# Kernel optimization log

Hardware: AMD Instinct MI355X
Metric: run time of the kernel (lower is better)

The kernel has to match this reference:

```python
import jax, jax.numpy as jnp
import numpy as np

H = 16          # attention_head_num
DH = 64         # attention_head_size
D = H * DH      # out_dim / model dim
SIZE_PER_HEAD = 64  # scaling denominator (init arg, used as sqrt divisor)


def setup_inputs() -> dict:
    key = jax.random.key(0)
    ks = jax.random.split(key, 12)
    B, S = 2, 2048
    scale = 1.0 / np.sqrt(D)
    inp = {
        "qx": jax.random.normal(ks[0], (B, S, D), dtype=jnp.float32),
        "kx": jax.random.normal(ks[1], (B, S, D), dtype=jnp.float32),
        "vx": jax.random.normal(ks[2], (B, S, D), dtype=jnp.float32),
        "Wq": jax.random.normal(ks[3], (D, D), dtype=jnp.float32) * scale,
        "bq": jnp.zeros((D,), dtype=jnp.float32),
        "Wk": jax.random.normal(ks[4], (D, D), dtype=jnp.float32) * scale,
        "bk": jnp.zeros((D,), dtype=jnp.float32),
        "Wv": jax.random.normal(ks[5], (D, D), dtype=jnp.float32) * scale,
        "bv": jnp.zeros((D,), dtype=jnp.float32),
        "Wo": jax.random.normal(ks[6], (D, D), dtype=jnp.float32) * scale,
        "bo": jnp.zeros((D,), dtype=jnp.float32),
    }
    return inp


def reference(qx, kx, vx, Wq, bq, Wk, bk, Wv, bv, Wo, bo):
    B, Sq, _ = qx.shape
    Sk = kx.shape[1]
    # QKV projections
    q = qx @ Wq + bq  # [B,Sq,D]
    k = kx @ Wk + bk  # [B,Sk,D]
    v = vx @ Wv + bv  # [B,Sk,D]
    # split heads -> [B,H,S,DH]
    q = q.reshape(B, Sq, H, DH).transpose(0, 2, 1, 3)
    k = k.reshape(B, Sk, H, DH).transpose(0, 2, 1, 3)
    v = v.reshape(B, Sk, H, DH).transpose(0, 2, 1, 3)
    # scores [B,H,Sq,Sk]; NOTE: original divides by sqrt(size_per_head)
    scores = jnp.einsum("bhqd,bhkd->bhqk", q, k) / jnp.sqrt(
        jnp.asarray(SIZE_PER_HEAD, dtype=q.dtype)
    )
    probs = jax.nn.softmax(scores, axis=-1)
    ctx = jnp.einsum("bhqk,bhkd->bhqd", probs, v)  # [B,H,Sq,DH]
    ctx = ctx.transpose(0, 2, 1, 3).reshape(B, Sq, D)
    return ctx @ Wo + bo
```

## Files before the change

kernel.cpp:

```cpp
#include <hip/hip_runtime.h>

typedef _Float16 half_t;
typedef _Float16 half8 __attribute__((ext_vector_type(8)));
typedef _Float16 half2v __attribute__((ext_vector_type(2)));
typedef __fp16 fp16x2 __attribute__((ext_vector_type(2)));
typedef float f32x16 __attribute__((ext_vector_type(16)));
typedef float f32x4v __attribute__((ext_vector_type(4)));
typedef unsigned uint2v __attribute__((ext_vector_type(2)));

#define MFMA32(A, B, C) __builtin_amdgcn_mfma_f32_32x32x16_f16(A, B, C, 0, 0, 0)

#if __has_builtin(__builtin_amdgcn_exp2f)
#define EXP2F(x) __builtin_amdgcn_exp2f(x)
#else
#define EXP2F(x) exp2f(x)
#endif

static constexpr int S = 2048;
static constexpr int D = 1024;
static constexpr float QSCALE = 0.18033688011112042f;


__device__ __forceinline__ void gload_lds16(const void* g, void* l) {
    __builtin_amdgcn_global_load_lds(
        (const __attribute__((address_space(1))) unsigned int*)g,
        (__attribute__((address_space(3))) unsigned int*)l, 16, 0, 0);
}

__global__ __launch_bounds__(256) void cvtw(
    const float* __restrict__ x0, const float* __restrict__ x1, const float* __restrict__ x2,
    const float* __restrict__ w0, const float* __restrict__ w1,
    const float* __restrict__ w2, const float* __restrict__ w3,
    half_t* __restrict__ o0, half_t* __restrict__ o1, half_t* __restrict__ o2,
    half_t* __restrict__ wt)
{
    __shared__ char sm[33280];
    int y = blockIdx.y;
    int t = threadIdx.x;
    if (y < 3) {
        float (*tile)[65] = (float(*)[65])sm;
        const float* src = (y == 0) ? x0 : (y == 1) ? x1 : x2;
        half_t* dst = (y == 0) ? o0 : (y == 1) ? o1 : o2;
        int mt = blockIdx.x >> 4, kt = blockIdx.x & 15;
        const float* sbase = src + (size_t)(mt * 128) * D + kt * 64;
        int rr = t >> 4, col = (t & 15) * 4;
#pragma unroll
        for (int p = 0; p < 8; ++p) {
            int row = rr + p * 16;
            f32x4v v = *(const f32x4v*)(sbase + (size_t)row * D + col);
            tile[row][col] = v[0]; tile[row][col + 1] = v[1];
            tile[row][col + 2] = v[2]; tile[row][col + 3] = v[3];
        }
        __syncthreads();
        int c = t >> 5, r0 = t & 31;
        half_t* dbase = dst + ((size_t)(mt * 16 + kt)) * 8192;
#pragma unroll
        for (int i = 0; i < 4; ++i) {
            int row = r0 + 32 * i;
            half8 h;
#pragma unroll
            for (int j = 0; j < 8; ++j) h[j] = (half_t)tile[row][c * 8 + j];
            *(half8*)(dbase + ((size_t)c * 128 + row) * 8) = h;
        }
    } else {
        float (*tile)[129] = (float(*)[129])sm;
        int w = blockIdx.x >> 7;
        const float* W = (w == 0) ? w0 : (w == 1) ? w1 : (w == 2) ? w2 : w3;
        int idx = blockIdx.x & 127;
        int nt = idx >> 4, kt = idx & 15;
        const float* sbase = W + (size_t)(kt * 64) * D + nt * 128;
        int kr = t >> 5, col = (t & 31) * 4;
#pragma unroll
        for (int p = 0; p < 8; ++p) {
            int k = kr + p * 8;
            f32x4v v = *(const f32x4v*)(sbase + (size_t)k * D + col);
            tile[k][col] = v[0]; tile[k][col + 1] = v[1];
            tile[k][col + 2] = v[2]; tile[k][col + 3] = v[3];
        }
        __syncthreads();
        int c = t >> 5, r0 = t & 31;
        half_t* dbase = wt + (size_t)w * 1048576 + ((size_t)(nt * 16 + kt)) * 8192;
#pragma unroll
        for (int i = 0; i < 4; ++i) {
            int n = r0 + 32 * i;
            half8 h;
#pragma unroll
            for (int j = 0; j < 8; ++j) h[j] = (half_t)tile[c * 8 + j][n];
            *(half8*)(dbase + ((size_t)c * 128 + n) * 8) = h;
        }
    }
}

__global__ __launch_bounds__(256, 4) void gemm_qkv(
    const half_t* __restrict__ a0, const half_t* __restrict__ a1, const half_t* __restrict__ a2,
    const half_t* __restrict__ wt,
    const float* __restrict__ b0, const float* __restrict__ b1, const float* __restrict__ b2,
    half_t* __restrict__ qh, half_t* __restrict__ kh, half_t* __restrict__ vt)
{
    __shared__ char smem[32768];
    half_t* As = (half_t*)smem;
    half_t* Bs = (half_t*)(smem + 16384);
    int z = blockIdx.z;
    const half_t* A = (z == 0) ? a0 : (z == 1) ? a1 : a2;
    const half_t* BT = wt + (size_t)z * 1048576;
    const float* bias = (z == 0) ? b0 : (z == 1) ? b1 : b2;
    int mt = blockIdx.x >> 3, nt8 = blockIdx.x & 7;
    int m0 = mt * 128, n0 = nt8 * 128;
    int tid = threadIdx.x, lane = tid & 63, wave = tid >> 6;
    int ml = lane & 31, hi = lane >> 5;
    int wm = (wave & 1) * 64, wn = (wave >> 1) * 64;

    f32x16 acc00 = {}, acc01 = {}, acc10 = {}, acc11 = {};

    for (int kt = 0; kt < 16; ++kt) {
        __syncthreads();
        const half_t* Aslab = A + ((size_t)(mt * 16 + kt)) * 8192;
        const half_t* Bslab = BT + ((size_t)(nt8 * 16 + kt)) * 8192;
#pragma unroll
        for (int j = 0; j < 4; ++j) {
            int s = wave * 4 + j;
            gload_lds16(Aslab + s * 512 + lane * 8, As + s * 512);
            gload_lds16(Bslab + s * 512 + lane * 8, Bs + s * 512);
        }
        __syncthreads();
#pragma unroll
        for (int ks = 0; ks < 4; ++ks) {
            int co = (2 * ks + hi) * 128;
            half8 af0 = *(const half8*)(As + (size_t)(co + wm + ml) * 8);
            half8 af1 = *(const half8*)(As + (size_t)(co + wm + 32 + ml) * 8);
            half8 bf0 = *(const half8*)(Bs + (size_t)(co + wn + ml) * 8);
            half8 bf1 = *(const half8*)(Bs + (size_t)(co + wn + 32 + ml) * 8);
            acc00 = MFMA32(af0, bf0, acc00);
            acc01 = MFMA32(af0, bf1, acc01);
            acc10 = MFMA32(af1, bf0, acc10);
            acc11 = MFMA32(af1, bf1, acc11);
        }
    }

    __syncthreads();
    half_t* buf = (half_t*)smem;
#pragma unroll
    for (int nt = 0; nt < 2; ++nt) {
        int nl = wn + nt * 32 + ml;
        float bv = bias[n0 + nl];
        int hh = nl >> 6, c = (nl >> 3) & 7, j = nl & 7, dd = nl & 63;
#pragma unroll
        for (int mt2 = 0; mt2 < 2; ++mt2) {
            f32x16 av = (mt2 == 0) ? (nt == 0 ? acc00 : acc01) : (nt == 0 ? acc10 : acc11);
#pragma unroll
            for (int r = 0; r < 16; ++r) {
                int rl = wm + mt2 * 32 + 4 * hi + (r & 3) + 8 * (r >> 2);
                float v = av[r] + bv;
                if (z == 0) v *= QSCALE;
                if (z <= 1) {
                    buf[((rl * 2 + hh) * 8 + (c ^ (rl & 7))) * 8 + j] = (half_t)v;
                } else {
                    int cc = rl >> 3, js = rl & 7;
                    buf[((dd * 2 + hh) * 16 + (cc ^ (dd & 7))) * 8 + js] = (half_t)v;
                }
            }
        }
    }
    __syncthreads();
    int bq_ = m0 >> 11, skt = (m0 >> 7) & 15, h0 = n0 >> 6;
    half_t* dstm = (z == 0) ? qh : (z == 1) ? kh : vt;
#pragma unroll
    for (int i = 0; i < 8; ++i) {
        int o = tid + 256 * i;
        int hh = o >> 10;
        half_t* gdst = dstm + ((size_t)(bq_ * 16 + h0 + hh)) * 131072 + (size_t)skt * 8192;
        half8 v8;
        int off;
        if (z <= 1) {
            int c = (o >> 7) & 7, r = o & 127;
            v8 = *(const half8*)(buf + (((r * 2 + hh) * 8 + (c ^ (r & 7))) * 8));
            off = (c * 128 + r) * 8;
        } else {
            int cc = (o >> 6) & 15, dd = o & 63;
            v8 = *(const half8*)(buf + (((dd * 2 + hh) * 16 + (cc ^ (dd & 7))) * 8));
            off = (cc * 64 + dd) * 8;
        }
        *(half8*)(gdst + off) = v8;
    }
}

__global__ __launch_bounds__(256, 4) void gemm_out(
    const half_t* __restrict__ A, const half_t* __restrict__ BT,
    const float* __restrict__ bias, float* __restrict__ out)
{
    __shared__ char smem[32768];
    half_t* As = (half_t*)smem;
    half_t* Bs = (half_t*)(smem + 16384);
    int mt = blockIdx.x >> 3, nt8 = blockIdx.x & 7;
    int m0 = mt * 128, n0 = nt8 * 128;
    int tid = threadIdx.x, lane = tid & 63, wave = tid >> 6;
    int ml = lane & 31, hi = lane >> 5;
    int wm = (wave & 1) * 64, wn = (wave >> 1) * 64;

    f32x16 acc00 = {}, acc01 = {}, acc10 = {}, acc11 = {};

    for (int kt = 0; kt < 16; ++kt) {
        __syncthreads();
        const half_t* Aslab = A + ((size_t)(mt * 16 + kt)) * 8192;
        const half_t* Bslab = BT + ((size_t)(nt8 * 16 + kt)) * 8192;
#pragma unroll
        for (int j = 0; j < 4; ++j) {
            int s = wave * 4 + j;
            gload_lds16(Aslab + s * 512 + lane * 8, As + s * 512);
            gload_lds16(Bslab + s * 512 + lane * 8, Bs + s * 512);
        }
        __syncthreads();
#pragma unroll
        for (int ks = 0; ks < 4; ++ks) {
            int co = (2 * ks + hi) * 128;
            half8 af0 = *(const half8*)(As + (size_t)(co + wm + ml) * 8);
            half8 af1 = *(const half8*)(As + (size_t)(co + wm + 32 + ml) * 8);
            half8 bf0 = *(const half8*)(Bs + (size_t)(co + wn + ml) * 8);
            half8 bf1 = *(const half8*)(Bs + (size_t)(co + wn + 32 + ml) * 8);
            acc00 = MFMA32(af0, bf0, acc00);
            acc01 = MFMA32(af0, bf1, acc01);
            acc10 = MFMA32(af1, bf0, acc10);
            acc11 = MFMA32(af1, bf1, acc11);
        }
    }

#pragma unroll
    for (int nt = 0; nt < 2; ++nt) {
        int n = n0 + wn + nt * 32 + ml;
        float bv = bias[n];
#pragma unroll
        for (int mt2 = 0; mt2 < 2; ++mt2) {
            f32x16 av = (mt2 == 0) ? (nt == 0 ? acc00 : acc01) : (nt == 0 ? acc10 : acc11);
            int rbase = m0 + wm + mt2 * 32 + 4 * hi;
#pragma unroll
            for (int r = 0; r < 16; ++r) {
                int row = rbase + (r & 3) + 8 * (r >> 2);
                out[(size_t)row * D + n] = av[r] + bv;
            }
        }
    }
}

__global__ __launch_bounds__(256, 2) void attn(
    const half_t* __restrict__ qh, const half_t* __restrict__ kh,
    const half_t* __restrict__ vt, half_t* __restrict__ ctx)
{
    __shared__ char smem[32768];
    half_t* Ks  = (half_t*)smem;
    half_t* VTs = (half_t*)(smem + 16384);

    int L = blockIdx.x;
    int slot = L >> 3;
    int bh = (L & 7) + 8 * (slot >> 4);
    int sq = slot & 15;
    int b = bh >> 4, h = bh & 15;

    int tid = threadIdx.x, lane = tid & 63, wave = tid >> 6;
    int ml = lane & 31, hi = lane >> 5;
    int qg = wave & 1, th = wave >> 1;
    const half_t* qslab = qh + (size_t)bh * 131072 + (size_t)sq * 8192;
    const half_t* khead = kh + (size_t)bh * 131072;
    const half_t* vhead = vt + (size_t)bh * 131072;

#pragma unroll
    for (int j = 0; j < 4; ++j) {
        int s = wave * 4 + j;
        gload_lds16(qslab + s * 512 + lane * 8, Ks + s * 512);
    }
    __syncthreads();
    half8 qf[2][4];
#pragma unroll
    for (int qs = 0; qs < 2; ++qs)
#pragma unroll
        for (int ks = 0; ks < 4; ++ks)
            qf[qs][ks] = *(const half8*)(Ks + ((size_t)((2 * ks + hi) * 128 + qg * 64 + qs * 32 + ml)) * 8);

    f32x16 oacc[2][2] = {};
    float lsum[2] = {0.0f, 0.0f};
    fp16x2 one2; one2.x = (__fp16)1.0f; one2.y = (__fp16)1.0f;

    for (int it = 0; it < 16; ++it) {
        __syncthreads();
        const half_t* kslab = khead + (size_t)it * 8192;
        const half_t* vslab = vhead + (size_t)it * 8192;
#pragma unroll
        for (int j = 0; j < 4; ++j) {
            int s = wave * 4 + j;
            gload_lds16(kslab + s * 512 + lane * 8, Ks + s * 512);
            gload_lds16(vslab + s * 512 + lane * 8, VTs + s * 512);
        }
        __syncthreads();

#pragma unroll
        for (int tt = 0; tt < 2; ++tt) {
            int t = th * 2 + tt;
            f32x16 s0 = {}, s1 = {};
#pragma unroll
            for (int ks = 0; ks < 4; ++ks) {
                half8 kf = *(const half8*)(Ks + ((size_t)((2 * ks + hi) * 128 + t * 32 + ml)) * 8);
                s0 = MFMA32(kf, qf[0][ks], s0);
                s1 = MFMA32(kf, qf[1][ks], s1);
            }
#pragma unroll
            for (int qs = 0; qs < 2; ++qs) {
                f32x16 sv = (qs == 0) ? s0 : s1;
                unsigned pkv[8];
                float ls = lsum[qs];
#pragma unroll
                for (int j = 0; j < 8; ++j) {
                    float pa = EXP2F(sv[2 * j] - 10.0f);
                    float pb = EXP2F(sv[2 * j + 1] - 10.0f);
#if __has_builtin(__builtin_amdgcn_cvt_pkrtz)
                    fp16x2 h2 = __builtin_amdgcn_cvt_pkrtz(pa, pb);
#else
                    fp16x2 h2; h2.x = (__fp16)pa; h2.y = (__fp16)pb;
#endif
                    pkv[j] = __builtin_bit_cast(unsigned, h2);
#if __has_builtin(__builtin_amdgcn_fdot2)
                    ls = __builtin_amdgcn_fdot2(h2, one2, ls, false);
#else
                    ls += pa + pb;
#endif
                }
                lsum[qs] = ls;
#pragma unroll
                for (int kp = 0; kp < 2; ++kp) {
                    union { unsigned u[4]; half8 h; } fr;
#if __has_builtin(__builtin_amdgcn_permlane32_swap)
                    uint2v w0 = __builtin_amdgcn_permlane32_swap(pkv[4 * kp + 0], pkv[4 * kp + 2], false, false);
                    uint2v w1 = __builtin_amdgcn_permlane32_swap(pkv[4 * kp + 1], pkv[4 * kp + 3], false, false);
                    fr.u[0] = w0.x; fr.u[1] = w1.x; fr.u[2] = w0.y; fr.u[3] = w1.y;
#else
                    unsigned e0 = pkv[4 * kp + 0], e1 = pkv[4 * kp + 1];
                    unsigned o0 = pkv[4 * kp + 2], o1 = pkv[4 * kp + 3];
                    unsigned s0u = hi ? e0 : o0, s1u = hi ? e1 : o1;
                    unsigned k0u = hi ? o0 : e0, k1u = hi ? o1 : e1;
                    unsigned r0 = __shfl_xor(s0u, 32, 64);
                    unsigned r1 = __shfl_xor(s1u, 32, 64);
                    fr.u[0] = hi ? r0 : k0u; fr.u[1] = hi ? r1 : k1u;
                    fr.u[2] = hi ? k0u : r0; fr.u[3] = hi ? k1u : r1;
#endif
#pragma unroll
                    for (int dt = 0; dt < 2; ++dt) {
                        half8 vf = *(const half8*)(VTs + ((size_t)((4 * t + 2 * kp + hi) * 64 + dt * 32 + ml)) * 8);
                        oacc[qs][dt] = MFMA32(fr.h, vf, oacc[qs][dt]);
                    }
                }
            }
        }
    }

    float lt[2];
    lt[0] = lsum[0] + __shfl_xor(lsum[0], 32, 64);
    lt[1] = lsum[1] + __shfl_xor(lsum[1], 32, 64);

    __syncthreads();
    float* OB = (float*)(smem + (size_t)qg * 16384);
    if (th == 1) {
#pragma unroll
        for (int qs = 0; qs < 2; ++qs)
#pragma unroll
            for (int dt = 0; dt < 2; ++dt)
#pragma unroll
                for (int r = 0; r < 16; ++r) {
                    int q = qs * 32 + 4 * hi + (r & 3) + 8 * (r >> 2);
                    OB[q * 64 + dt * 32 + ml] = oacc[qs][dt][r];
                }
    }
    __syncthreads();
    if (th == 0) {
#pragma unroll
        for (int qs = 0; qs < 2; ++qs)
#pragma unroll
            for (int dt = 0; dt < 2; ++dt)
#pragma unroll
                for (int r = 0; r < 16; ++r) {
                    int q = qs * 32 + 4 * hi + (r & 3) + 8 * (r >> 2);
                    oacc[qs][dt][r] += OB[q * 64 + dt * 32 + ml];
                }
    }
    __syncthreads();
    float* Lbuf = (float*)smem;
    if (th == 1 && hi == 0) {
        Lbuf[qg * 64 + ml] = lt[0];
        Lbuf[qg * 64 + 32 + ml] = lt[1];
    }
    __syncthreads();
    if (th == 0 && hi == 0) {
        Lbuf[qg * 64 + ml] += lt[0];
        Lbuf[qg * 64 + 32 + ml] += lt[1];
    }
    __syncthreads();
    if (th == 0) {
        half_t* cslab = ctx + ((size_t)((b * 16 + sq) * 16 + h)) * 8192;
#pragma unroll
        for (int qs = 0; qs < 2; ++qs)
#pragma unroll
            for (int dt = 0; dt < 2; ++dt)
#pragma unroll
                for (int r = 0; r < 16; ++r) {
                    int q = qs * 32 + 4 * hi + (r & 3) + 8 * (r >> 2);
                    int d = dt * 32 + ml;
                    float linv = __builtin_amdgcn_rcpf(Lbuf[qg * 64 + q]);
                    cslab[((d >> 3) * 128 + qg * 64 + q) * 8 + (d & 7)] =
                        (half_t)(oacc[qs][dt][r] * linv);
                }
    }
}

extern "C" void kernel_launch(void* const* d_in, const int* in_sizes, int n_in,
                              void* d_out, int out_size, void* d_ws, size_t ws_size,
                              hipStream_t stream)
{
    const float* qx = (const float*)d_in[0];
    const float* kx = (const float*)d_in[1];
    const float* vx = (const float*)d_in[2];
    const float* Wq = (const float*)d_in[3];
    const float* bq = (const float*)d_in[4];
    const float* Wk = (const float*)d_in[5];
    const float* bk = (const float*)d_in[6];
    const float* Wv = (const float*)d_in[7];
    const float* bv = (const float*)d_in[8];
    const float* Wo = (const float*)d_in[9];
    const float* bo = (const float*)d_in[10];
    float* out = (float*)d_out;

    half_t* ws = (half_t*)d_ws;
    const size_t NT = (size_t)4096 * 1024;
    half_t* qxh = ws;
    half_t* kxh = qxh + NT;
    half_t* vxh = kxh + NT;
    half_t* wt = vxh + NT;
    half_t* qh = wt + (size_t)4 * 1048576;
    half_t* kh = qh + NT;
    half_t* vtr = kh + NT;
    half_t* ctx = vtr + NT;

    cvtw<<<dim3(512, 4), 256, 0, stream>>>(qx, kx, vx, Wq, Wk, Wv, Wo, qxh, kxh, vxh, wt);
    gemm_qkv<<<dim3(256, 1, 3), 256, 0, stream>>>(qxh, kxh, vxh, wt, bq, bk, bv, qh, kh, vtr);
    attn<<<dim3(512, 1, 1), 256, 0, stream>>>(qh, kh, vtr, ctx);
    gemm_out<<<dim3(256, 1, 1), 256, 0, stream>>>(ctx, wt + (size_t)3 * 1048576, bo, out);
}
```

Measured before the change: 227.5 us.

## Double-buffer K/V tiles in attention and swizzle GEMM block order

The attention kernel now uses 64KB of LDS to double-buffer K and V tiles. The loads for the next key tile are issued before computing on the current one, and one barrier per iteration replaces two. Q gets its own LDS region, and the first K/V tile is loaded together with it. Both GEMM kernels also remap block indices so that consecutive blocks share B column tiles and spread across M, aiming for better L2 reuse; the larger LDS footprint may limit occupancy.

```diff
diff --git a/kernel.cpp b/kernel.cpp
--- a/kernel.cpp
+++ b/kernel.cpp
@@ -2,7 +2,6 @@
 
 typedef _Float16 half_t;
 typedef _Float16 half8 __attribute__((ext_vector_type(8)));
-typedef _Float16 half2v __attribute__((ext_vector_type(2)));
 typedef __fp16 fp16x2 __attribute__((ext_vector_type(2)));
 typedef float f32x16 __attribute__((ext_vector_type(16)));
 typedef float f32x4v __attribute__((ext_vector_type(4)));
@@ -104,7 +103,10 @@
     const half_t* A = (z == 0) ? a0 : (z == 1) ? a1 : a2;
     const half_t* BT = wt + (size_t)z * 1048576;
     const float* bias = (z == 0) ? b0 : (z == 1) ? b1 : b2;
-    int mt = blockIdx.x >> 3, nt8 = blockIdx.x & 7;
+    int L = blockIdx.x;
+    int w = L >> 3;
+    int mt = (L & 7) * 4 + (w & 3);
+    int nt8 = w >> 2;
     int m0 = mt * 128, n0 = nt8 * 128;
     int tid = threadIdx.x, lane = tid & 63, wave = tid >> 6;
     int ml = lane & 31, hi = lane >> 5;
@@ -191,7 +193,10 @@
     __shared__ char smem[32768];
     half_t* As = (half_t*)smem;
     half_t* Bs = (half_t*)(smem + 16384);
-    int mt = blockIdx.x >> 3, nt8 = blockIdx.x & 7;
+    int L = blockIdx.x;
+    int w = L >> 3;
+    int mt = (L & 7) * 4 + (w & 3);
+    int nt8 = w >> 2;
     int m0 = mt * 128, n0 = nt8 * 128;
     int tid = threadIdx.x, lane = tid & 63, wave = tid >> 6;
     int ml = lane & 31, hi = lane >> 5;
@@ -245,15 +250,13 @@
     const half_t* __restrict__ qh, const half_t* __restrict__ kh,
     const half_t* __restrict__ vt, half_t* __restrict__ ctx)
 {
-    __shared__ char smem[32768];
-    half_t* Ks  = (half_t*)smem;
-    half_t* VTs = (half_t*)(smem + 16384);
+    __shared__ char smem[65536];
 
     int L = blockIdx.x;
     int slot = L >> 3;
     int bh = (L & 7) + 8 * (slot >> 4);
     int sq = slot & 15;
-    int b = bh >> 4, h = bh & 15;
+    int b_ = bh >> 4, h = bh & 15;
 
     int tid = threadIdx.x, lane = tid & 63, wave = tid >> 6;
     int ml = lane & 31, hi = lane >> 5;
@@ -262,34 +265,50 @@
     const half_t* khead = kh + (size_t)bh * 131072;
     const half_t* vhead = vt + (size_t)bh * 131072;
 
-#pragma unroll
-    for (int j = 0; j < 4; ++j) {
-        int s = wave * 4 + j;
-        gload_lds16(qslab + s * 512 + lane * 8, Ks + s * 512);
+    {
+        half_t* QB = (half_t*)(smem + 32768);
+        half_t* K0 = (half_t*)(smem);
+        half_t* V0 = (half_t*)(smem + 16384);
+#pragma unroll
+        for (int j = 0; j < 4; ++j) {
+            int s = wave * 4 + j;
+            gload_lds16(qslab + s * 512 + lane * 8, QB + s * 512);
+            gload_lds16(khead + s * 512 + lane * 8, K0 + s * 512);
+            gload_lds16(vhead + s * 512 + lane * 8, V0 + s * 512);
+        }
     }
     __syncthreads();
     half8 qf[2][4];
-#pragma unroll
-    for (int qs = 0; qs < 2; ++qs)
-#pragma unroll
-        for (int ks = 0; ks < 4; ++ks)
-            qf[qs][ks] = *(const half8*)(Ks + ((size_t)((2 * ks + hi) * 128 + qg * 64 + qs * 32 + ml)) * 8);
+    {
+        half_t* QB = (half_t*)(smem + 32768);
+#pragma unroll
+        for (int qs = 0; qs < 2; ++qs)
+#pragma unroll
+            for (int ks = 0; ks < 4; ++ks)
+                qf[qs][ks] = *(const half8*)(QB + ((size_t)((2 * ks + hi) * 128 + qg * 64 + qs * 32 + ml)) * 8);
+    }
+    __syncthreads();
 
     f32x16 oacc[2][2] = {};
     float lsum[2] = {0.0f, 0.0f};
     fp16x2 one2; one2.x = (__fp16)1.0f; one2.y = (__fp16)1.0f;
 
     for (int it = 0; it < 16; ++it) {
-        __syncthreads();
-        const half_t* kslab = khead + (size_t)it * 8192;
-        const half_t* vslab = vhead + (size_t)it * 8192;
-#pragma unroll
-        for (int j = 0; j < 4; ++j) {
-            int s = wave * 4 + j;
-            gload_lds16(kslab + s * 512 + lane * 8, Ks + s * 512);
-            gload_lds16(vslab + s * 512 + lane * 8, VTs + s * 512);
-        }
-        __syncthreads();
+        int bb = it & 1;
+        if (it < 15) {
+            const half_t* kslab = khead + (size_t)(it + 1) * 8192;
+            const half_t* vslab = vhead + (size_t)(it + 1) * 8192;
+            half_t* Kd = (half_t*)(smem + (bb ^ 1) * 32768);
+            half_t* Vd = (half_t*)(smem + 16384 + (bb ^ 1) * 32768);
+#pragma unroll
+            for (int j = 0; j < 4; ++j) {
+                int s = wave * 4 + j;
+                gload_lds16(kslab + s * 512 + lane * 8, Kd + s * 512);
+                gload_lds16(vslab + s * 512 + lane * 8, Vd + s * 512);
+            }
+        }
+        half_t* Ks  = (half_t*)(smem + bb * 32768);
+        half_t* VTs = (half_t*)(smem + 16384 + bb * 32768);
 
 #pragma unroll
         for (int tt = 0; tt < 2; ++tt) {
@@ -348,13 +367,13 @@
                 }
             }
         }
+        __syncthreads();
     }
 
     float lt[2];
     lt[0] = lsum[0] + __shfl_xor(lsum[0], 32, 64);
     lt[1] = lsum[1] + __shfl_xor(lsum[1], 32, 64);
 
-    __syncthreads();
     float* OB = (float*)(smem + (size_t)qg * 16384);
     if (th == 1) {
 #pragma unroll
@@ -392,7 +411,7 @@
     }
     __syncthreads();
     if (th == 0) {
-        half_t* cslab = ctx + ((size_t)((b * 16 + sq) * 16 + h)) * 8192;
+        half_t* cslab = ctx + ((size_t)((b_ * 16 + sq) * 16 + h)) * 8192;
 #pragma unroll
         for (int qs = 0; qs < 2; ++qs)
 #pragma unroll
```

Measured after the change: 214.9 us. 1.06x faster.
